# Kernel tuning notes

Hardware: AMD Instinct MI355X
Metric: run time of the kernel (lower is better)

Reference implementation:

```python
import jax, jax.numpy as jnp
import numpy as np

INF = 10000000000000.0
HEADS = 12
HEAD_SIZE = 64

def _rope_tables(seqlen, dim):
    inv_freq = 1.0 / (10000.0 ** (jnp.arange(0, dim, 2, dtype=jnp.float32) / dim))
    t = jnp.arange(seqlen, dtype=jnp.float32)
    freqs = t[:, None] * inv_freq[None, :]            # [S, d/2]
    # unsqueeze_dim=-2 -> [S, 1, d/2] to broadcast over heads
    return jnp.sin(freqs)[:, None, :], jnp.cos(freqs)[:, None, :]

def _apply_rope(t, sin, cos):
    # t: [B, S, H, D]; sin/cos: [S, 1, D/2]
    t1, t2 = t[..., 0::2], t[..., 1::2]
    out = jnp.stack([t1 * cos - t2 * sin, t1 * sin + t2 * cos], axis=-1)
    return out.reshape(t.shape)

def setup_inputs() -> dict:
    key = jax.random.key(0)
    k1, k2 = jax.random.split(key)
    B, S, Hd = 32, 512, 1024
    x = jax.random.normal(k1, (B, S, Hd), dtype=jnp.float32)
    W = jax.random.normal(k2, (Hd, HEADS * 2 * HEAD_SIZE), dtype=jnp.float32) * (1.0 / np.sqrt(Hd))
    b = jnp.zeros((HEADS * 2 * HEAD_SIZE,), dtype=jnp.float32)
    attention_mask = jnp.ones((B, S), dtype=jnp.int32)
    return {"x": x, "W": W, "b": b, "attention_mask": attention_mask}

def reference(x, W, b, attention_mask):
    B, S, _ = x.shape
    proj = x @ W + b                                   # [B, S, H*2*D]
    proj = proj.reshape(B, S, HEADS, 2, HEAD_SIZE)
    qw, kw = proj[..., 0, :], proj[..., 1, :]          # [B, S, H, D]
    sin, cos = _rope_tables(S, HEAD_SIZE)
    qw = _apply_rope(qw, sin, cos)
    kw = _apply_rope(kw, sin, cos)
    logits = jnp.einsum('bmhd,bnhd->bhmn', qw, kw)     # [B, H, S, S]
    am = attention_mask.astype(logits.dtype)
    pad_mask = 1.0 - am[:, None, None, :] * am[:, None, :, None]
    logits = logits - pad_mask * INF
    idx = jnp.arange(S)
    tril = (idx[:, None] > idx[None, :]).astype(logits.dtype)  # strictly lower triangle
    logits = logits - tril * INF
    return logits / (HEAD_SIZE ** 0.5)
```

## Files before the change

### kernel.cpp

```cpp
#include <hip/hip_runtime.h>
#include <hip/hip_bf16.h>
#include <cstdint>

#define HEADS 12
#define HEAD_SIZE 64
#define SEQ 512
#define HD 1024
#define NPROJ 1536
#define INF_VAL 1e13f

typedef __attribute__((ext_vector_type(8))) __bf16 bf16x8;
typedef __attribute__((ext_vector_type(4))) float f32x4;

__device__ __forceinline__ unsigned short f2bf(float f) {
    unsigned u = __float_as_uint(f);
    u += 0x7fffu + ((u >> 16) & 1u);
    return (unsigned short)(u >> 16);
}

__device__ __forceinline__ void gl_lds16(const unsigned short* g, unsigned short* l) {
    __builtin_amdgcn_global_load_lds(
        (const __attribute__((address_space(1))) unsigned int*)g,
        (__attribute__((address_space(3))) unsigned int*)l, 16, 0, 0);
}

__global__ void __launch_bounds__(256) convert_x(const float* __restrict__ x,
                                                 unsigned short* __restrict__ xb) {
    const int i = blockIdx.x * 256 + threadIdx.x;
    const float4* src = (const float4*)x;
    float4 v0 = src[i * 2 + 0];
    float4 v1 = src[i * 2 + 1];
    uint4 p;
    p.x = f2bf(v0.x) | ((unsigned)f2bf(v0.y) << 16);
    p.y = f2bf(v0.z) | ((unsigned)f2bf(v0.w) << 16);
    p.z = f2bf(v1.x) | ((unsigned)f2bf(v1.y) << 16);
    p.w = f2bf(v1.z) | ((unsigned)f2bf(v1.w) << 16);
    ((uint4*)xb)[i] = p;
}

__global__ void __launch_bounds__(256) transpose_cast_w(const float* __restrict__ W,
                                                        unsigned short* __restrict__ Wt) {
    __shared__ unsigned short tile[64][65];
    const int bx = blockIdx.x;
    const int k0 = (bx & 15) * 64;
    const int n0 = (bx >> 4) * 64;
    const int t = threadIdx.x;
    const int tr = t >> 4;
    const int tc = (t & 15) * 4;
#pragma unroll
    for (int i = 0; i < 4; ++i) {
        int kk = tr + i * 16;
        float4 v = *(const float4*)&W[(size_t)(k0 + kk) * NPROJ + n0 + tc];
        tile[kk][tc + 0] = f2bf(v.x);
        tile[kk][tc + 1] = f2bf(v.y);
        tile[kk][tc + 2] = f2bf(v.z);
        tile[kk][tc + 3] = f2bf(v.w);
    }
    __syncthreads();
#pragma unroll
    for (int i = 0; i < 4; ++i) {
        int nn = tr + i * 16;
        ushort4 o;
        o.x = tile[tc + 0][nn];
        o.y = tile[tc + 1][nn];
        o.z = tile[tc + 2][nn];
        o.w = tile[tc + 3][nn];
        *(ushort4*)&Wt[(size_t)(n0 + nn) * HD + k0 + tc] = o;
    }
}

__global__ void __launch_bounds__(256) rope_table(float2* __restrict__ tab) {
    const int e = blockIdx.x * 256 + threadIdx.x;
    const int srow = e >> 5;
    const int fi = e & 31;
    float invf = __expf(-(float)fi * (0.03125f * 9.210340371976184f));
    float theta = (float)srow * invf;
    float sv, cv;
    __sincosf(theta, &sv, &cv);
    tab[e] = make_float2(sv, cv);
}

__global__ void __launch_bounds__(256) gemm1_rope(const unsigned short* __restrict__ xb,
                                                  const unsigned short* __restrict__ Wt,
                                                  const float* __restrict__ bias,
                                                  const float2* __restrict__ tab,
                                                  unsigned short* __restrict__ qws,
                                                  unsigned short* __restrict__ kws) {
    __shared__ __align__(16) char smem[32768];
    unsigned short* Alds = (unsigned short*)smem;
    unsigned short* Blds = (unsigned short*)(smem + 16384);

    const int bx0 = blockIdx.x;
    const int bx = (bx0 & 7) * 192 + (bx0 >> 3);
    const int tile_m = bx / HEADS;
    const int h = bx - tile_m * HEADS;
    const int m0 = tile_m * 128;
    const int n0 = h * 128;

    const int t = threadIdx.x;
    const int w = t >> 6;
    const int lane = t & 63;
    const int wm = w >> 1;
    const int wn = w & 1;
    const int c16 = lane & 15;
    const int quad = lane >> 4;

    const int srow0 = w * 32 + (lane >> 3);
    const int scel = (lane & 7) * 8;
    const unsigned short* gA[4];
    const unsigned short* gB[4];
    unsigned short* lA[4];
    unsigned short* lB[4];
#pragma unroll
    for (int j = 0; j < 4; ++j) {
        gA[j] = xb + (size_t)(m0 + srow0 + j * 8) * HD + scel;
        gB[j] = Wt + (size_t)(n0 + srow0 + j * 8) * HD + scel;
        lA[j] = Alds + (srow0 + j * 8) * 64 + scel;
        lB[j] = Blds + (srow0 + j * 8) * 64 + scel;
    }

    f32x4 acc[4][4];
#pragma unroll
    for (int i = 0; i < 4; ++i)
#pragma unroll
        for (int j = 0; j < 4; ++j) acc[i][j] = (f32x4){0.f, 0.f, 0.f, 0.f};

    for (int kt = 0; kt < HD; kt += 64) {
#pragma unroll
        for (int j = 0; j < 4; ++j) {
            gl_lds16(gA[j] + kt, lA[j]);
            gl_lds16(gB[j] + kt, lB[j]);
        }
        __syncthreads();

#pragma unroll
        for (int ks = 0; ks < 2; ++ks) {
            bf16x8 af[4], bfr[4];
#pragma unroll
            for (int mi = 0; mi < 4; ++mi)
                af[mi] = *(const bf16x8*)((char*)Alds + (wm * 64 + mi * 16 + c16) * 128 + ks * 64 + quad * 16);
#pragma unroll
            for (int ni = 0; ni < 4; ++ni)
                bfr[ni] = *(const bf16x8*)((char*)Blds + (wn * 64 + ni * 16 + c16) * 128 + ks * 64 + quad * 16);
#pragma unroll
            for (int mi = 0; mi < 4; ++mi)
#pragma unroll
                for (int ni = 0; ni < 4; ++ni)
                    acc[mi][ni] = __builtin_amdgcn_mfma_f32_16x16x32_bf16(af[mi], bfr[ni], acc[mi][ni], 0, 0, 0);
        }
        __syncthreads();
    }

    float bv[4];
#pragma unroll
    for (int ni = 0; ni < 4; ++ni) bv[ni] = bias[n0 + wn * 64 + ni * 16 + c16];

    const int bb = m0 >> 9;
    const int sbase = m0 & (SEQ - 1);
    const int odd = c16 & 1;
    const float sgn = odd ? 1.f : -1.f;
    unsigned short* outp = wn ? kws : qws;
    const size_t obase = ((size_t)(bb * HEADS + h) * SEQ + sbase) * HEAD_SIZE;

#pragma unroll
    for (int mi = 0; mi < 4; ++mi) {
#pragma unroll
        for (int ni = 0; ni < 4; ++ni) {
            const int d = ni * 16 + c16;
            const int fi = d >> 1;
#pragma unroll
            for (int r = 0; r < 4; ++r) {
                const int srow = wm * 64 + mi * 16 + quad * 4 + r;
                float v = acc[mi][ni][r] + bv[ni];
                float p = __shfl_xor(v, 1, 64);
                float2 sc = tab[(sbase + srow) * 32 + fi];
                float o = v * sc.y + sgn * p * sc.x;
                float o2 = __shfl_xor(o, 1, 64);
                if (!odd) {
                    unsigned pk;
                    asm("v_cvt_pk_bf16_f32 %0, %1, %2" : "=v"(pk) : "v"(o), "v"(o2));
                    *(unsigned*)&outp[obase + (size_t)srow * HEAD_SIZE + d] = pk;
                }
            }
        }
    }
}

__global__ void __launch_bounds__(256) gemm2_mask(const unsigned short* __restrict__ qws,
                                                  const unsigned short* __restrict__ kws,
                                                  const int* __restrict__ am,
                                                  float* __restrict__ out) {
    const int lin = blockIdx.y * 16 + blockIdx.x;
    const int swz = (lin & 7) * 768 + (lin >> 3);
    const int bh = swz >> 4;
    const int tile = swz & 15;
    const int b = bh / HEADS;
    const int tm = (tile >> 2) * 128;
    const int tn = (tile & 3) * 128;
    const int t = threadIdx.x;
    const int w = t >> 6, lane = t & 63;
    const int wm = w >> 1, wn = w & 1;
    const int c16 = lane & 15, quad = lane >> 4;

    const unsigned short* qp = qws + (size_t)bh * SEQ * HEAD_SIZE;
    const unsigned short* kp = kws + (size_t)bh * SEQ * HEAD_SIZE;

    f32x4 acc[4][4];
#pragma unroll
    for (int i = 0; i < 4; ++i)
#pragma unroll
        for (int j = 0; j < 4; ++j) acc[i][j] = (f32x4){0.f, 0.f, 0.f, 0.f};

#pragma unroll
    for (int ks = 0; ks < 2; ++ks) {
        bf16x8 af[4], bfr[4];
#pragma unroll
        for (int mi = 0; mi < 4; ++mi)
            af[mi] = *(const bf16x8*)(qp + (size_t)(tm + wm * 64 + mi * 16 + c16) * HEAD_SIZE
                                         + ks * 32 + quad * 8);
#pragma unroll
        for (int ni = 0; ni < 4; ++ni)
            bfr[ni] = *(const bf16x8*)(kp + (size_t)(tn + wn * 64 + ni * 16 + c16) * HEAD_SIZE
                                          + ks * 32 + quad * 8);
#pragma unroll
        for (int mi = 0; mi < 4; ++mi)
#pragma unroll
            for (int ni = 0; ni < 4; ++ni)
                acc[mi][ni] = __builtin_amdgcn_mfma_f32_16x16x32_bf16(bfr[ni], af[mi], acc[mi][ni], 0, 0, 0);
    }

    const int* amb = am + b * SEQ;
    float ammv[4];
#pragma unroll
    for (int mi = 0; mi < 4; ++mi) ammv[mi] = (float)amb[tm + wm * 64 + mi * 16 + c16];

#pragma unroll
    for (int ni = 0; ni < 4; ++ni) {
        const int nb = tn + wn * 64 + ni * 16 + quad * 4;
        const int4 a4 = *(const int4*)&amb[nb];
        const float an0 = (float)a4.x, an1 = (float)a4.y, an2 = (float)a4.z, an3 = (float)a4.w;
#pragma unroll
        for (int mi = 0; mi < 4; ++mi) {
            const int m = tm + wm * 64 + mi * 16 + c16;
            const float amm = ammv[mi];
            f32x4 o;
            o[0] = (acc[mi][ni][0] - ((1.0f - amm * an0) + ((m > nb + 0) ? 1.0f : 0.0f)) * INF_VAL) * 0.125f;
            o[1] = (acc[mi][ni][1] - ((1.0f - amm * an1) + ((m > nb + 1) ? 1.0f : 0.0f)) * INF_VAL) * 0.125f;
            o[2] = (acc[mi][ni][2] - ((1.0f - amm * an2) + ((m > nb + 2) ? 1.0f : 0.0f)) * INF_VAL) * 0.125f;
            o[3] = (acc[mi][ni][3] - ((1.0f - amm * an3) + ((m > nb + 3) ? 1.0f : 0.0f)) * INF_VAL) * 0.125f;
            __builtin_nontemporal_store(o, (f32x4*)&out[((size_t)bh * SEQ + m) * SEQ + nb]);
        }
    }
}

extern "C" void kernel_launch(void* const* d_in, const int* in_sizes, int n_in,
                              void* d_out, int out_size, void* d_ws, size_t ws_size,
                              hipStream_t stream) {
    (void)in_sizes; (void)n_in; (void)out_size; (void)ws_size;
    const float* x = (const float*)d_in[0];
    const float* W = (const float*)d_in[1];
    const float* bias = (const float*)d_in[2];
    const int* am = (const int*)d_in[3];
    float* out = (float*)d_out;

    unsigned short* Wt  = (unsigned short*)d_ws;
    unsigned short* qws = (unsigned short*)((char*)d_ws + 3145728);
    unsigned short* kws = (unsigned short*)((char*)d_ws + 3145728 + 25165824);
    unsigned short* xb  = (unsigned short*)((char*)d_ws + 3145728 + 2 * 25165824);
    float2* tab = (float2*)((char*)d_ws + 3145728 + 2 * 25165824 + 33554432);

    hipLaunchKernelGGL(convert_x, dim3(8192), dim3(256), 0, stream, x, xb);
    hipLaunchKernelGGL(transpose_cast_w, dim3(384), dim3(256), 0, stream, W, Wt);
    hipLaunchKernelGGL(rope_table, dim3(64), dim3(256), 0, stream, tab);
    hipLaunchKernelGGL(gemm1_rope, dim3(128 * HEADS), dim3(256), 0, stream, xb, Wt, bias, tab, qws, kws);
    hipLaunchKernelGGL(gemm2_mask, dim3(16, 32 * HEADS), dim3(256), 0, stream, qws, kws, am, out);
}
```

Baseline: 597.6 us.

## Double-buffer GEMM1 LDS tiles with XOR swizzle; drop block-index swizzles

```diff
diff --git a/kernel.cpp b/kernel.cpp
--- a/kernel.cpp
+++ b/kernel.cpp
@@ -86,12 +86,9 @@
                                                   const float2* __restrict__ tab,
                                                   unsigned short* __restrict__ qws,
                                                   unsigned short* __restrict__ kws) {
-    __shared__ __align__(16) char smem[32768];
-    unsigned short* Alds = (unsigned short*)smem;
-    unsigned short* Blds = (unsigned short*)(smem + 16384);
-
-    const int bx0 = blockIdx.x;
-    const int bx = (bx0 & 7) * 192 + (bx0 >> 3);
+    __shared__ __align__(16) unsigned short smem[32768];
+
+    const int bx = blockIdx.x;
     const int tile_m = bx / HEADS;
     const int h = bx - tile_m * HEADS;
     const int m0 = tile_m * 128;
@@ -105,18 +102,17 @@
     const int c16 = lane & 15;
     const int quad = lane >> 4;
 
-    const int srow0 = w * 32 + (lane >> 3);
-    const int scel = (lane & 7) * 8;
+    const int sr = lane >> 3;
+    const int scel = (((lane & 7) ^ sr) * 8);
     const unsigned short* gA[4];
     const unsigned short* gB[4];
-    unsigned short* lA[4];
-    unsigned short* lB[4];
+    int lofs[4];
 #pragma unroll
     for (int j = 0; j < 4; ++j) {
-        gA[j] = xb + (size_t)(m0 + srow0 + j * 8) * HD + scel;
-        gB[j] = Wt + (size_t)(n0 + srow0 + j * 8) * HD + scel;
-        lA[j] = Alds + (srow0 + j * 8) * 64 + scel;
-        lB[j] = Blds + (srow0 + j * 8) * 64 + scel;
+        const int row = j * 32 + w * 8 + sr;
+        gA[j] = xb + (size_t)(m0 + row) * HD + scel;
+        gB[j] = Wt + (size_t)(n0 + row) * HD + scel;
+        lofs[j] = j * 2048 + w * 512 + lane * 8;
     }
 
     f32x4 acc[4][4];
@@ -125,23 +121,36 @@
 #pragma unroll
         for (int j = 0; j < 4; ++j) acc[i][j] = (f32x4){0.f, 0.f, 0.f, 0.f};
 
-    for (int kt = 0; kt < HD; kt += 64) {
-#pragma unroll
-        for (int j = 0; j < 4; ++j) {
-            gl_lds16(gA[j] + kt, lA[j]);
-            gl_lds16(gB[j] + kt, lB[j]);
-        }
-        __syncthreads();
-
+#pragma unroll
+    for (int j = 0; j < 4; ++j) {
+        gl_lds16(gA[j], smem + lofs[j]);
+        gl_lds16(gB[j], smem + 8192 + lofs[j]);
+    }
+    __syncthreads();
+
+    const int swq = (quad ^ (c16 & 7)) * 16;
+
+    for (int kt = 0; kt < 16; ++kt) {
+        const int cur = kt & 1;
+        const char* base = (const char*)(smem + cur * 16384);
+        if (kt < 15) {
+            const int nk = (kt + 1) * 64;
+            unsigned short* nb = smem + (cur ^ 1) * 16384;
+#pragma unroll
+            for (int j = 0; j < 4; ++j) {
+                gl_lds16(gA[j] + nk, nb + lofs[j]);
+                gl_lds16(gB[j] + nk, nb + 8192 + lofs[j]);
+            }
+        }
 #pragma unroll
         for (int ks = 0; ks < 2; ++ks) {
             bf16x8 af[4], bfr[4];
 #pragma unroll
             for (int mi = 0; mi < 4; ++mi)
-                af[mi] = *(const bf16x8*)((char*)Alds + (wm * 64 + mi * 16 + c16) * 128 + ks * 64 + quad * 16);
+                af[mi] = *(const bf16x8*)(base + (wm * 64 + mi * 16 + c16) * 128 + (swq ^ (ks * 64)));
 #pragma unroll
             for (int ni = 0; ni < 4; ++ni)
-                bfr[ni] = *(const bf16x8*)((char*)Blds + (wn * 64 + ni * 16 + c16) * 128 + ks * 64 + quad * 16);
+                bfr[ni] = *(const bf16x8*)(base + 16384 + (wn * 64 + ni * 16 + c16) * 128 + (swq ^ (ks * 64)));
 #pragma unroll
             for (int mi = 0; mi < 4; ++mi)
 #pragma unroll
@@ -190,13 +199,10 @@
                                                   const unsigned short* __restrict__ kws,
                                                   const int* __restrict__ am,
                                                   float* __restrict__ out) {
-    const int lin = blockIdx.y * 16 + blockIdx.x;
-    const int swz = (lin & 7) * 768 + (lin >> 3);
-    const int bh = swz >> 4;
-    const int tile = swz & 15;
+    const int bh = blockIdx.y;
     const int b = bh / HEADS;
-    const int tm = (tile >> 2) * 128;
-    const int tn = (tile & 3) * 128;
+    const int tm = (blockIdx.x >> 2) * 128;
+    const int tn = (blockIdx.x & 3) * 128;
     const int t = threadIdx.x;
     const int w = t >> 6, lane = t & 63;
     const int wm = w >> 1, wn = w & 1;
```

Measured after the change: 585.0 us. 1.02x faster.
